# Kernel tuning notes

Hardware: AMD Instinct MI355X
Metric: run time of the kernel (lower is better)

## Reference

```python
import jax, jax.numpy as jnp
import numpy as np

B, N, NP, K, C_IN, C, H = 16, 4096, 1024, 32, 128, 256, 4
C_G = C_IN + 3  # grouped feature dim (use_xyz concat of relative coords)
EPS = 1e-3      # keras LayerNormalization default epsilon


def setup_inputs() -> dict:
    key = jax.random.key(0)
    ks = jax.random.split(key, 16)
    s = 0.05
    return {
        "xyz": jax.random.normal(ks[0], (B, N, 3), jnp.float32),
        "newxyz": jax.random.normal(ks[1], (B, NP, 3), jnp.float32),
        "feature_input": jax.random.normal(ks[2], (B, N, C_IN), jnp.float32),
        "w_qkv": jax.random.normal(ks[3], (C_G, 3 * C), jnp.float32) * s,
        "proj_w": jax.random.normal(ks[4], (C, C), jnp.float32) * s,
        "proj_b": jnp.zeros((C,), jnp.float32),
        "dense_w": jax.random.normal(ks[5], (C_G, C), jnp.float32) * s,
        "dense_b": jnp.zeros((C,), jnp.float32),
        "fc1_w": jax.random.normal(ks[6], (C, 2 * C), jnp.float32) * s,
        "fc1_b": jnp.zeros((2 * C,), jnp.float32),
        "fc2_w": jax.random.normal(ks[7], (2 * C, C), jnp.float32) * s,
        "fc2_b": jnp.zeros((C,), jnp.float32),
        "n1_g": jnp.ones((C_G,), jnp.float32),
        "n1_b": jnp.zeros((C_G,), jnp.float32),
        "n2_g": jnp.ones((C,), jnp.float32),
        "n2_b": jnp.zeros((C,), jnp.float32),
        "group_num": K,
        "training": True,
    }


def _layernorm(x, g, b):
    m = jnp.mean(x, axis=-1, keepdims=True)
    v = jnp.mean(jnp.square(x - m), axis=-1, keepdims=True)
    return (x - m) * jax.lax.rsqrt(v + EPS) * g + b


def _sample_and_group(newxyz, group_num, xyz, feats):
    # squared pairwise distances (B, NP, N)
    d2 = (jnp.sum(newxyz**2, -1)[:, :, None]
          - 2.0 * jnp.einsum('bpc,bnc->bpn', newxyz, xyz)
          + jnp.sum(xyz**2, -1)[:, None, :])
    _, idx = jax.lax.top_k(-d2, group_num)            # (B, NP, K) nearest
    b_idx = jnp.arange(newxyz.shape[0])[:, None, None]
    grouped_xyz = xyz[b_idx, idx] - newxyz[:, :, None, :]   # (B, NP, K, 3)
    grouped_feat = feats[b_idx, idx]                        # (B, NP, K, C_IN)
    return jnp.concatenate([grouped_xyz, grouped_feat], axis=-1)


def _self_attention(x, w_qkv, proj_w, proj_b):
    b, n, k = x.shape[0], x.shape[1], x.shape[2]
    d = C // H
    qkv = jnp.einsum('bnkc,cd->bnkd', x, w_qkv)
    qkv = qkv.reshape(b, n, k, 3, H, d)
    qkv = jnp.transpose(qkv, (3, 0, 1, 4, 2, 5))      # (3, B, NP, H, K, d)
    q, kk, v = qkv[0], qkv[1], qkv[2]
    qm = jnp.max(q, axis=-2, keepdims=True)           # (B, NP, H, 1, d)
    attn = jnp.einsum('bnhqd,bnhkd->bnhqk', qm, kk) * (C ** -0.5)
    attn = jax.nn.softmax(attn, axis=-1)
    out = jnp.einsum('bnhqk,bnhkd->bnhqd', attn, v)[..., 0, :]  # (B, NP, H, d)
    out = out.reshape(b, n, C)
    return jax.nn.relu(out @ proj_w + proj_b)


def reference(xyz, newxyz, feature_input, w_qkv, proj_w, proj_b, dense_w,
              dense_b, fc1_w, fc1_b, fc2_w, fc2_b, n1_g, n1_b, n2_g, n2_b,
              group_num, training):
    gf = _sample_and_group(newxyz, group_num, xyz, feature_input)  # (B,NP,K,C_G)
    feat = _self_attention(_layernorm(gf, n1_g, n1_b), w_qkv, proj_w, proj_b)
    feat = feat + jax.nn.relu(jnp.max(gf, axis=-2) @ dense_w + dense_b)
    f2 = _layernorm(feat, n2_g, n2_b)
    f2 = jax.nn.relu(f2 @ fc1_w + fc1_b)
    f2 = f2 @ fc2_w + fc2_b
    return f2 + feat
```

## Files before the change

kernel.cpp:

```cpp
#include <hip/hip_runtime.h>
#include <hip/hip_bf16.h>

typedef __hip_bfloat16 bf16;

#define Bn   16
#define Nn   4096
#define NPn  1024
#define Kn   32
#define CINn 128
#define CGn  131
#define Cn   256
#define Hn   4
#define KPAD 160
#define XBS  168
#define XFS2 136
#define GFS  136

typedef __attribute__((ext_vector_type(8))) short frag_ab;
typedef __attribute__((ext_vector_type(4))) float frag_cd;

__device__ __forceinline__ float b2f(bf16 x) { return __bfloat162float(x); }
__device__ __forceinline__ bf16  f2b(float x) { return __float2bfloat16(x); }
__device__ __forceinline__ short f2bs(float x) {
  union { bf16 h; short s; } u; u.h = __float2bfloat16(x); return u.s;
}
__device__ __forceinline__ float bs2f(short s) {
  union { short v; bf16 h; } u; u.v = s; return __bfloat162float(u.h);
}
__device__ __forceinline__ unsigned f2ord(float f) {
  unsigned u = __float_as_uint(f);
  return u ^ ((u >> 31) ? 0xffffffffu : 0x80000000u);
}

__global__ __launch_bounds__(256) void knn_kernel(const float* __restrict__ xyz,
                                                  const float* __restrict__ newxyz,
                                                  int* __restrict__ idx_out) {
  constexpr int CAP = 2048;
  __shared__ unsigned long long tmin[256];
  __shared__ __align__(16) unsigned long long cand[CAP + 4];
  __shared__ unsigned long long wtau[4];
  __shared__ unsigned long long wred[4];
  __shared__ int scnt;
  const int bp  = blockIdx.x;
  const int b   = bp >> 10;
  const int tid = threadIdx.x;
  const float qx = newxyz[bp*3 + 0];
  const float qy = newxyz[bp*3 + 1];
  const float qz = newxyz[bp*3 + 2];
  const float sn = __fadd_rn(__fadd_rn(__fmul_rn(qx,qx), __fmul_rn(qy,qy)),
                             __fmul_rn(qz,qz));
  const float* xb = xyz + (size_t)b * Nn * 3;
  unsigned long long key[16];
  unsigned long long lmin = ~0ull;
  #pragma unroll
  for (int s = 0; s < 16; ++s) {
    const int n = s*256 + tid;
    const float xx = xb[n*3 + 0];
    const float xy = xb[n*3 + 1];
    const float xz = xb[n*3 + 2];
    const float sx  = __fadd_rn(__fadd_rn(__fmul_rn(xx,xx), __fmul_rn(xy,xy)),
                                __fmul_rn(xz,xz));
    const float dot = __fadd_rn(__fadd_rn(__fmul_rn(qx,xx), __fmul_rn(qy,xy)),
                                __fmul_rn(qz,xz));
    const float d2 = __fadd_rn(__fsub_rn(sn, __fmul_rn(2.0f, dot)), sx);
    key[s] = ((unsigned long long)f2ord(d2) << 32) | (unsigned)n;
    if (key[s] < lmin) lmin = key[s];
  }
  const int lane = tid & 63, wv = tid >> 6;

  if (tid == 0) scnt = 0;
  tmin[tid] = lmin;
  __syncthreads();

  {
    const unsigned long long* wt = &tmin[wv * 64];
    int rk = 0;
    #pragma unroll 8
    for (int j = 0; j < 64; ++j) rk += (wt[j] < lmin) ? 1 : 0;
    if (rk == 31) wtau[wv] = lmin;
  }
  __syncthreads();
  unsigned long long tau = wtau[0];
  if (wtau[1] < tau) tau = wtau[1];
  if (wtau[2] < tau) tau = wtau[2];
  if (wtau[3] < tau) tau = wtau[3];

  #pragma unroll
  for (int s = 0; s < 16; ++s) {
    if (key[s] <= tau) {
      const int p = atomicAdd(&scnt, 1);
      if (p < CAP) cand[p] = key[s];
    }
  }
  __syncthreads();
  const int m = scnt;

  if (m <= CAP) {
    if (tid < 4) cand[m + tid] = ~0ull;
    __syncthreads();
    const int m4 = (m + 3) & ~3;
    for (int t = tid; t < m; t += 256) {
      const unsigned long long mykey = cand[t];
      int r = 0;
      for (int j = 0; j < m4; j += 4) {
        r += (cand[j+0] < mykey) ? 1 : 0;
        r += (cand[j+1] < mykey) ? 1 : 0;
        r += (cand[j+2] < mykey) ? 1 : 0;
        r += (cand[j+3] < mykey) ? 1 : 0;
      }
      if (r < Kn) idx_out[(size_t)bp*Kn + r] = (int)(mykey & 0xffffffffu);
    }
  } else {
    for (int s = 0; s < Kn; ++s) {
      unsigned long long mm = lmin;
      #pragma unroll
      for (int d = 32; d; d >>= 1) {
        const unsigned lo = __shfl_xor((unsigned)(mm & 0xffffffffu), d, 64);
        const unsigned hi = __shfl_xor((unsigned)(mm >> 32), d, 64);
        const unsigned long long o = ((unsigned long long)hi << 32) | lo;
        if (o < mm) mm = o;
      }
      if (lane == 0) wred[wv] = mm;
      __syncthreads();
      unsigned long long best = wred[0];
      if (wred[1] < best) best = wred[1];
      if (wred[2] < best) best = wred[2];
      if (wred[3] < best) best = wred[3];
      __syncthreads();
      const int n = (int)(best & 0xffffffffu);
      if (tid == 0) idx_out[(size_t)bp*Kn + s] = n;
      if ((n & 255) == tid) {
        const int slot = n >> 8;
        #pragma unroll
        for (int t = 0; t < 16; ++t) if (t == slot) key[t] = ~0ull;
        unsigned long long m2 = ~0ull;
        #pragma unroll
        for (int t = 0; t < 16; ++t) if (key[t] < m2) m2 = key[t];
        lmin = m2;
      }
    }
  }
}

__global__ __launch_bounds__(256) void wprep_all_kernel(
    const float* __restrict__ w_qkv, const float* __restrict__ proj_w,
    const float* __restrict__ dense_w, const float* __restrict__ fc1_w,
    const float* __restrict__ fc2_w, short* __restrict__ o_qkv,
    short* __restrict__ o_proj, short* __restrict__ o_dense,
    short* __restrict__ o_fc1, short* __restrict__ o_fc2) {
  const int blk = blockIdx.x;
  const float* W; short* out; int K, N, nnt, remap, base;
  if      (blk <  480) { W=w_qkv;   out=o_qkv;   K=CGn; N=768; nnt=48; remap=1; base=0;    }
  else if (blk <  736) { W=proj_w;  out=o_proj;  K=Cn;  N=256; nnt=16; remap=0; base=480;  }
  else if (blk <  896) { W=dense_w; out=o_dense; K=CGn; N=256; nnt=16; remap=1; base=736;  }
  else if (blk < 1408) { W=fc1_w;   out=o_fc1;   K=Cn;  N=512; nnt=32; remap=0; base=896;  }
  else                 { W=fc2_w;   out=o_fc2;   K=512; N=256; nnt=16; remap=0; base=1408; }
  const int t = (blk - base) * 256 + threadIdx.x;
  const int j    = t & 7;
  const int lane = (t >> 3) & 63;
  const int nt   = (t >> 9) % nnt;
  const int kt   = (t >> 9) / nnt;
  const int k = kt*32 + (lane >> 4)*8 + j;
  const int n = nt*16 + (lane & 15);
  int krow = k;
  if (remap) krow = (k < 128) ? k + 3 : k - 128;
  out[t] = (k < K) ? f2bs(W[(size_t)krow*N + n]) : (short)0;
}

__global__ __launch_bounds__(256, 3) void fused_attn_kernel(
    const float* __restrict__ xyz, const float* __restrict__ newxyz,
    const float* __restrict__ featin, const short* __restrict__ wfrag,
    const float* __restrict__ n1g, const float* __restrict__ n1b,
    const int* __restrict__ idx, bf16* __restrict__ attnout,
    bf16* __restrict__ gfmax) {
  __shared__ __align__(16) short Xs[64 * XBS];
  __shared__ float sg[CGn], sb[CGn];
  __shared__ int sidx[64];
  const int bp0 = blockIdx.x * 2;
  const int b   = bp0 >> 10;
  const int tid = threadIdx.x;
  if (tid < 64) {
    int n = idx[(size_t)bp0*Kn + tid];
    sidx[tid] = ((unsigned)n < (unsigned)Nn) ? n : 0;
  }
  if (tid < CGn) {
    const int rj = (tid < 128) ? tid + 3 : tid - 128;
    sg[tid] = n1g[rj];
    sb[tid] = n1b[rj];
  }
  __syncthreads();
  const int kk = tid >> 3, sub = tid & 7;
  float4 r[2][4];
  float ex[2] = {0.f, 0.f};
  #pragma unroll
  for (int p = 0; p < 2; ++p) {
    const int row = p*32 + kk;
    const float* frow = featin + ((size_t)b*Nn + sidx[row])*CINn;
    #pragma unroll
    for (int i = 0; i < 4; ++i) r[p][i] = *(const float4*)(frow + sub*4 + 32*i);
    if (sub < 3)
      ex[p] = xyz[((size_t)b*Nn + sidx[row])*3 + sub] - newxyz[(bp0+p)*3 + sub];
  }
  #pragma unroll
  for (int p = 0; p < 2; ++p) {
    const int row = p*32 + kk;
    #pragma unroll
    for (int i = 0; i < 4; ++i) {
      short4 s4 = { f2bs(r[p][i].x), f2bs(r[p][i].y), f2bs(r[p][i].z), f2bs(r[p][i].w) };
      *(short4*)&Xs[row*XFS2 + sub*4 + 32*i] = s4;
    }
    if (sub < 3) Xs[row*XFS2 + 128 + sub] = f2bs(ex[p]);
  }
  float mean[2], rstd[2];
  #pragma unroll
  for (int p = 0; p < 2; ++p) {
    float s = ex[p], s2 = ex[p]*ex[p];
    #pragma unroll
    for (int i = 0; i < 4; ++i) {
      s  += r[p][i].x + r[p][i].y + r[p][i].z + r[p][i].w;
      s2 += r[p][i].x*r[p][i].x + r[p][i].y*r[p][i].y
          + r[p][i].z*r[p][i].z + r[p][i].w*r[p][i].w;
    }
    s  += __shfl_xor(s, 1, 64);  s  += __shfl_xor(s, 2, 64);  s  += __shfl_xor(s, 4, 64);
    s2 += __shfl_xor(s2, 1, 64); s2 += __shfl_xor(s2, 2, 64); s2 += __shfl_xor(s2, 4, 64);
    mean[p] = s * (1.0f/CGn);
    const float var = s2 * (1.0f/CGn) - mean[p]*mean[p];
    rstd[p] = rsqrtf(var + 1e-3f);
  }
  __syncthreads();
  #pragma unroll
  for (int p = 0; p < 2; ++p) {
    if (tid < GFS) {
      float m = 0.f;
      if (tid < CGn) {
        m = -1e30f;
        #pragma unroll
        for (int k2 = 0; k2 < Kn; ++k2)
          m = fmaxf(m, bs2f(Xs[(p*32 + k2)*XFS2 + tid]));
      }
      gfmax[(size_t)(bp0+p)*GFS + tid] = f2b(m);
    }
  }
  __syncthreads();
  #pragma unroll
  for (int p = 0; p < 2; ++p) {
    const int row = p*32 + kk;
    #pragma unroll
    for (int i = 0; i < 4; ++i) {
      const float4 g4 = *(const float4*)&sg[sub*4 + 32*i];
      const float4 b4 = *(const float4*)&sb[sub*4 + 32*i];
      short4 s4;
      s4.x = f2bs((r[p][i].x - mean[p])*rstd[p]*g4.x + b4.x);
      s4.y = f2bs((r[p][i].y - mean[p])*rstd[p]*g4.y + b4.y);
      s4.z = f2bs((r[p][i].z - mean[p])*rstd[p]*g4.z + b4.z);
      s4.w = f2bs((r[p][i].w - mean[p])*rstd[p]*g4.w + b4.w);
      *(short4*)&Xs[row*XBS + sub*4 + 32*i] = s4;
    }
    if (sub < 3)
      Xs[row*XBS + 128 + sub] = f2bs((ex[p] - mean[p])*rstd[p]*sg[128+sub] + sb[128+sub]);
  }
  #pragma unroll
  for (int u = 0; u < 8; ++u) {
    const int e = u*256 + tid;
    const int row = e >> 5, jj = 131 + (e & 31);
    if (jj < 160) Xs[row*XBS + jj] = 0;
  }
  __syncthreads();
  const int lane = tid & 63, w = tid >> 6;
  const int col = lane & 15, quad = lane >> 4;
  float qm[2][4], aw[2][2][4], inv[2];
  {
    #pragma unroll 1
    for (int half = 0; half < 2; ++half) {
      frag_cd acc[2][4] = {};
      for (int kt = 0; kt < 5; ++kt) {
        const int ko = kt*32 + quad*8;
        frag_ab a[4];
        #pragma unroll
        for (int mt = 0; mt < 4; ++mt)
          a[mt] = *(const frag_ab*)&Xs[(mt*16 + col)*XBS + ko];
        #pragma unroll
        for (int ntl = 0; ntl < 2; ++ntl) {
          const int nt = w*4 + half*2 + ntl;
          const frag_ab bfr = *(const frag_ab*)(wfrag + ((size_t)(kt*48 + nt)*64 + lane)*8);
          #pragma unroll
          for (int mt = 0; mt < 4; ++mt)
            acc[ntl][mt] = __builtin_amdgcn_mfma_f32_16x16x32_bf16(a[mt], bfr, acc[ntl][mt], 0, 0, 0);
        }
      }
      #pragma unroll
      for (int p = 0; p < 2; ++p)
        #pragma unroll
        for (int ntl = 0; ntl < 2; ++ntl) {
          float m = -1e30f;
          #pragma unroll
          for (int mtl = 0; mtl < 2; ++mtl)
            #pragma unroll
            for (int rr = 0; rr < 4; ++rr) m = fmaxf(m, acc[ntl][p*2+mtl][rr]);
          m = fmaxf(m, __shfl_xor(m, 16, 64));
          m = fmaxf(m, __shfl_xor(m, 32, 64));
          qm[p][half*2 + ntl] = m;
        }
    }
  }
  {
    float pp[2][2][4] = {};
    #pragma unroll 1
    for (int half = 0; half < 2; ++half) {
      frag_cd acc[2][4] = {};
      for (int kt = 0; kt < 5; ++kt) {
        const int ko = kt*32 + quad*8;
        frag_ab a[4];
        #pragma unroll
        for (int mt = 0; mt < 4; ++mt)
          a[mt] = *(const frag_ab*)&Xs[(mt*16 + col)*XBS + ko];
        #pragma unroll
        for (int ntl = 0; ntl < 2; ++ntl) {
          const int nt = 16 + w*4 + half*2 + ntl;
          const frag_ab bfr = *(const frag_ab*)(wfrag + ((size_t)(kt*48 + nt)*64 + lane)*8);
          #pragma unroll
          for (int mt = 0; mt < 4; ++mt)
            acc[ntl][mt] = __builtin_amdgcn_mfma_f32_16x16x32_bf16(a[mt], bfr, acc[ntl][mt], 0, 0, 0);
        }
      }
      #pragma unroll
      for (int p = 0; p < 2; ++p)
        #pragma unroll
        for (int mtl = 0; mtl < 2; ++mtl)
          #pragma unroll
          for (int rr = 0; rr < 4; ++rr) {
            #pragma unroll
            for (int ntl = 0; ntl < 2; ++ntl)
              pp[p][mtl][rr] = fmaf(qm[p][half*2 + ntl], acc[ntl][p*2+mtl][rr], pp[p][mtl][rr]);
          }
    }
    #pragma unroll
    for (int p = 0; p < 2; ++p) {
      float lg[2][4];
      #pragma unroll
      for (int mtl = 0; mtl < 2; ++mtl)
        #pragma unroll
        for (int rr = 0; rr < 4; ++rr) {
          float v = pp[p][mtl][rr];
          #pragma unroll
          for (int d = 1; d < 16; d <<= 1) v += __shfl_xor(v, d, 64);
          lg[mtl][rr] = v * 0.0625f;
        }
      float mx = -1e30f;
      #pragma unroll
      for (int mtl = 0; mtl < 2; ++mtl)
        #pragma unroll
        for (int rr = 0; rr < 4; ++rr) mx = fmaxf(mx, lg[mtl][rr]);
      mx = fmaxf(mx, __shfl_xor(mx, 16, 64));
      mx = fmaxf(mx, __shfl_xor(mx, 32, 64));
      float ssum = 0.f;
      #pragma unroll
      for (int mtl = 0; mtl < 2; ++mtl)
        #pragma unroll
        for (int rr = 0; rr < 4; ++rr) { aw[p][mtl][rr] = expf(lg[mtl][rr] - mx); ssum += aw[p][mtl][rr]; }
      ssum += __shfl_xor(ssum, 16, 64);
      ssum += __shfl_xor(ssum, 32, 64);
      inv[p] = 1.f / ssum;
    }
  }
  {
    #pragma unroll 1
    for (int half = 0; half < 2; ++half) {
      frag_cd acc[2][4] = {};
      for (int kt = 0; kt < 5; ++kt) {
        const int ko = kt*32 + quad*8;
        frag_ab a[4];
        #pragma unroll
        for (int mt = 0; mt < 4; ++mt)
          a[mt] = *(const frag_ab*)&Xs[(mt*16 + col)*XBS + ko];
        #pragma unroll
        for (int ntl = 0; ntl < 2; ++ntl) {
          const int nt = 32 + w*4 + half*2 + ntl;
          const frag_ab bfr = *(const frag_ab*)(wfrag + ((size_t)(kt*48 + nt)*64 + lane)*8);
          #pragma unroll
          for (int mt = 0; mt < 4; ++mt)
            acc[ntl][mt] = __builtin_amdgcn_mfma_f32_16x16x32_bf16(a[mt], bfr, acc[ntl][mt], 0, 0, 0);
        }
      }
      #pragma unroll
      for (int p = 0; p < 2; ++p)
        #pragma unroll
        for (int ntl = 0; ntl < 2; ++ntl) {
          float o = 0.f;
          #pragma unroll
          for (int mtl = 0; mtl < 2; ++mtl)
            #pragma unroll
            for (int rr = 0; rr < 4; ++rr) o = fmaf(aw[p][mtl][rr], acc[ntl][p*2+mtl][rr], o);
          o += __shfl_xor(o, 16, 64);
          o += __shfl_xor(o, 32, 64);
          if (quad == 0)
            attnout[(size_t)(bp0+p)*Cn + w*64 + (half*2 + ntl)*16 + col] = f2b(o * inv[p]);
        }
    }
  }
}

template<bool RELU, bool ADD_S, bool OUT_BF16>
__global__ __launch_bounds__(256) void mfma_gemm_kernel(
    const bf16* __restrict__ A, int lda, int Ka,
    const short* __restrict__ Wf, int nnt_total, int N,
    const float* __restrict__ bias, const bf16* __restrict__ S,
    void* __restrict__ Dv) {
  __shared__ __align__(16) short As[64*40];
  const int m0 = blockIdx.y * 64;
  const int n0 = blockIdx.x * 128;
  const int tid = threadIdx.x, lane = tid & 63, w = tid >> 6;
  const int col = lane & 15, quad = lane >> 4;
  const int row = tid >> 2, c8 = (tid & 3) * 8;
  frag_cd acc[4][2] = {};
  const int nkt = (Ka + 31) >> 5;
  for (int kt = 0; kt < nkt; ++kt) {
    const int k0 = kt*32 + c8;
    frag_ab av = {0,0,0,0,0,0,0,0};
    if (k0 + 8 <= Ka)
      av = *(const frag_ab*)((const short*)A + (size_t)(m0+row)*lda + k0);
    __syncthreads();
    *(frag_ab*)&As[row*40 + c8] = av;
    __syncthreads();
    frag_ab afr[4];
    #pragma unroll
    for (int mt = 0; mt < 4; ++mt)
      afr[mt] = *(const frag_ab*)&As[(mt*16 + col)*40 + quad*8];
    #pragma unroll
    for (int ntl = 0; ntl < 2; ++ntl) {
      const int nt = (n0 >> 4) + w*2 + ntl;
      const frag_ab bfr = *(const frag_ab*)(Wf + ((size_t)(kt*nnt_total + nt)*64 + lane)*8);
      #pragma unroll
      for (int mt = 0; mt < 4; ++mt)
        acc[mt][ntl] = __builtin_amdgcn_mfma_f32_16x16x32_bf16(afr[mt], bfr, acc[mt][ntl], 0, 0, 0);
    }
  }
  #pragma unroll
  for (int ntl = 0; ntl < 2; ++ntl) {
    const int n = n0 + w*32 + ntl*16 + col;
    const float bv = bias[n];
    #pragma unroll
    for (int mt = 0; mt < 4; ++mt) {
      #pragma unroll
      for (int r = 0; r < 4; ++r) {
        const int m = m0 + mt*16 + quad*4 + r;
        float v = acc[mt][ntl][r] + bv;
        if (RELU) v = fmaxf(v, 0.f);
        if (ADD_S) v += b2f(S[(size_t)m*N + n]);
        if (OUT_BF16) ((bf16*)Dv)[(size_t)m*N + n] = f2b(v);
        else          ((float*)Dv)[(size_t)m*N + n] = v;
      }
    }
  }
}

__global__ __launch_bounds__(256) void dual_gemm_kernel(
    const bf16* __restrict__ A1, const short* __restrict__ W1,
    const bf16* __restrict__ A2, const short* __restrict__ W2,
    const float* __restrict__ b1, const float* __restrict__ b2,
    bf16* __restrict__ D) {
  __shared__ __align__(16) short As[64*40];
  const int m0 = blockIdx.y * 64;
  const int n0 = blockIdx.x * 128;
  const int tid = threadIdx.x, lane = tid & 63, w = tid >> 6;
  const int col = lane & 15, quad = lane >> 4;
  const int row = tid >> 2, c8 = (tid & 3) * 8;
  frag_cd acc1[4][2] = {}, acc2[4][2] = {};
  for (int kt = 0; kt < 8; ++kt) {
    const frag_ab av = *(const frag_ab*)((const short*)A1 + (size_t)(m0+row)*Cn + kt*32 + c8);
    __syncthreads();
    *(frag_ab*)&As[row*40 + c8] = av;
    __syncthreads();
    frag_ab afr[4];
    #pragma unroll
    for (int mt = 0; mt < 4; ++mt)
      afr[mt] = *(const frag_ab*)&As[(mt*16 + col)*40 + quad*8];
    #pragma unroll
    for (int ntl = 0; ntl < 2; ++ntl) {
      const int nt = (n0 >> 4) + w*2 + ntl;
      const frag_ab bfr = *(const frag_ab*)(W1 + ((size_t)(kt*16 + nt)*64 + lane)*8);
      #pragma unroll
      for (int mt = 0; mt < 4; ++mt)
        acc1[mt][ntl] = __builtin_amdgcn_mfma_f32_16x16x32_bf16(afr[mt], bfr, acc1[mt][ntl], 0, 0, 0);
    }
  }
  for (int kt = 0; kt < 5; ++kt) {
    const int k0 = kt*32 + c8;
    frag_ab av = {0,0,0,0,0,0,0,0};
    if (k0 + 8 <= GFS)
      av = *(const frag_ab*)((const short*)A2 + (size_t)(m0+row)*GFS + k0);
    __syncthreads();
    *(frag_ab*)&As[row*40 + c8] = av;
    __syncthreads();
    frag_ab afr[4];
    #pragma unroll
    for (int mt = 0; mt < 4; ++mt)
      afr[mt] = *(const frag_ab*)&As[(mt*16 + col)*40 + quad*8];
    #pragma unroll
    for (int ntl = 0; ntl < 2; ++ntl) {
      const int nt = (n0 >> 4) + w*2 + ntl;
      const frag_ab bfr = *(const frag_ab*)(W2 + ((size_t)(kt*16 + nt)*64 + lane)*8);
      #pragma unroll
      for (int mt = 0; mt < 4; ++mt)
        acc2[mt][ntl] = __builtin_amdgcn_mfma_f32_16x16x32_bf16(afr[mt], bfr, acc2[mt][ntl], 0, 0, 0);
    }
  }
  #pragma unroll
  for (int ntl = 0; ntl < 2; ++ntl) {
    const int n = n0 + w*32 + ntl*16 + col;
    const float bv1 = b1[n], bv2 = b2[n];
    #pragma unroll
    for (int mt = 0; mt < 4; ++mt) {
      #pragma unroll
      for (int r = 0; r < 4; ++r) {
        const int m = m0 + mt*16 + quad*4 + r;
        const float v = fmaxf(acc1[mt][ntl][r] + bv1, 0.f)
                      + fmaxf(acc2[mt][ntl][r] + bv2, 0.f);
        D[(size_t)m*Cn + n] = f2b(v);
      }
    }
  }
}

__global__ __launch_bounds__(256) void ln2_kernel(const bf16* __restrict__ feat,
                                                  const float* __restrict__ g,
                                                  const float* __restrict__ b,
                                                  bf16* __restrict__ out) {
  const int r = blockIdx.x*4 + (threadIdx.x >> 6), lane = threadIdx.x & 63;
  float vv[4];
  #pragma unroll
  for (int c = 0; c < 4; ++c) vv[c] = b2f(feat[(size_t)r*Cn + lane*4 + c]);
  float s  = vv[0] + vv[1] + vv[2] + vv[3];
  float s2 = vv[0]*vv[0] + vv[1]*vv[1] + vv[2]*vv[2] + vv[3]*vv[3];
  #pragma unroll
  for (int d = 32; d; d >>= 1) { s += __shfl_xor(s, d, 64); s2 += __shfl_xor(s2, d, 64); }
  const float mean = s * (1.f/256.f);
  const float var  = s2 * (1.f/256.f) - mean*mean;
  const float rstd = rsqrtf(var + 1e-3f);
  #pragma unroll
  for (int c = 0; c < 4; ++c) {
    const int cc = lane*4 + c;
    out[(size_t)r*Cn + cc] = f2b((vv[c] - mean)*rstd*g[cc] + b[cc]);
  }
}

extern "C" void kernel_launch(void* const* d_in, const int* in_sizes, int n_in,
                              void* d_out, int out_size, void* d_ws, size_t ws_size,
                              hipStream_t stream) {
  const float* xyz     = (const float*)d_in[0];
  const float* newxyz  = (const float*)d_in[1];
  const float* featin  = (const float*)d_in[2];
  const float* w_qkv   = (const float*)d_in[3];
  const float* proj_w  = (const float*)d_in[4];
  const float* proj_b  = (const float*)d_in[5];
  const float* dense_w = (const float*)d_in[6];
  const float* dense_b = (const float*)d_in[7];
  const float* fc1_w   = (const float*)d_in[8];
  const float* fc1_b   = (const float*)d_in[9];
  const float* fc2_w   = (const float*)d_in[10];
  const float* fc2_b   = (const float*)d_in[11];
  const float* n1g     = (const float*)d_in[12];
  const float* n1b     = (const float*)d_in[13];
  const float* n2g     = (const float*)d_in[14];
  const float* n2b     = (const float*)d_in[15];

  char*  ws     = (char*)d_ws;
  short* wqkv   = (short*)(ws + 0);
  short* wproj  = (short*)(ws + 245760);
  short* wdense = (short*)(ws + 376832);
  short* wfc1   = (short*)(ws + 458752);
  short* wfc2   = (short*)(ws + 720896);
  bf16*  featB  = (bf16*)(ws + 1048576);
  bf16*  attnA  = (bf16*)(ws + 9437184);
  bf16*  gfmax  = (bf16*)(ws + 17825792);
  int*   idxws  = (int*) (ws + 22282240);
  bf16*  fc1out = (bf16*)(ws + 24379392);

  const int M = Bn * NPn;

  knn_kernel<<<dim3(M), dim3(256), 0, stream>>>(xyz, newxyz, idxws);
  wprep_all_kernel<<<dim3(1920), dim3(256), 0, stream>>>(
      w_qkv, proj_w, dense_w, fc1_w, fc2_w, wqkv, wproj, wdense, wfc1, wfc2);

  fused_attn_kernel<<<dim3(M/2), dim3(256), 0, stream>>>(
      xyz, newxyz, featin, wqkv, n1g, n1b, idxws, attnA, gfmax);
  dual_gemm_kernel<<<dim3(2, M/64), dim3(256), 0, stream>>>(
      attnA, wproj, gfmax, wdense, proj_b, dense_b, featB);
  ln2_kernel<<<dim3(M/4), dim3(256), 0, stream>>>(featB, n2g, n2b, attnA);
  mfma_gemm_kernel<true, false, true><<<dim3(4, M/64), dim3(256), 0, stream>>>(
      attnA, Cn, Cn, wfc1, 32, 512, fc1_b, (const bf16*)nullptr, fc1out);
  mfma_gemm_kernel<false, true, false><<<dim3(2, M/64), dim3(256), 0, stream>>>(
      fc1out, 512, 512, wfc2, 16, Cn, fc2_b, featB, d_out);
}
```

Before: 435.3 us.

## Precompute padded xyz with squared norms, tighten KNN threshold, stage raw features in LDS

Adds a prep kernel that packs xyz into float4 with the precomputed squared norm, so each KNN block does one vector load per point and skips the norm arithmetic. The KNN candidate threshold now uses the rank-15 thread minimum per wave instead of rank-31, which shrinks the candidate set, and a fallback path handles the case where fewer than K candidates survive. The fused attention kernel keeps the raw bf16 features in a separate LDS buffer instead of holding fp32 registers across barriers, which drops one barrier but adds LDS use and lowers LayerNorm input precision to bf16. The xyzw buffer reuses the fc1out workspace region.

```diff
diff --git a/kernel.cpp b/kernel.cpp
--- a/kernel.cpp
+++ b/kernel.cpp
@@ -32,7 +32,18 @@
   return u ^ ((u >> 31) ? 0xffffffffu : 0x80000000u);
 }
 
-__global__ __launch_bounds__(256) void knn_kernel(const float* __restrict__ xyz,
+__global__ __launch_bounds__(256) void xyzw_prep_kernel(
+    const float* __restrict__ xyz, float4* __restrict__ xyzw) {
+  const int i = blockIdx.x * 256 + threadIdx.x;
+  const float x = xyz[i*3 + 0];
+  const float y = xyz[i*3 + 1];
+  const float z = xyz[i*3 + 2];
+  const float sx = __fadd_rn(__fadd_rn(__fmul_rn(x,x), __fmul_rn(y,y)),
+                             __fmul_rn(z,z));
+  xyzw[i] = make_float4(x, y, z, sx);
+}
+
+__global__ __launch_bounds__(256) void knn_kernel(const float4* __restrict__ xyzw,
                                                   const float* __restrict__ newxyz,
                                                   int* __restrict__ idx_out) {
   constexpr int CAP = 2048;
@@ -49,20 +60,16 @@
   const float qz = newxyz[bp*3 + 2];
   const float sn = __fadd_rn(__fadd_rn(__fmul_rn(qx,qx), __fmul_rn(qy,qy)),
                              __fmul_rn(qz,qz));
-  const float* xb = xyz + (size_t)b * Nn * 3;
+  const float4* xb = xyzw + (size_t)b * Nn;
   unsigned long long key[16];
   unsigned long long lmin = ~0ull;
   #pragma unroll
   for (int s = 0; s < 16; ++s) {
     const int n = s*256 + tid;
-    const float xx = xb[n*3 + 0];
-    const float xy = xb[n*3 + 1];
-    const float xz = xb[n*3 + 2];
-    const float sx  = __fadd_rn(__fadd_rn(__fmul_rn(xx,xx), __fmul_rn(xy,xy)),
-                                __fmul_rn(xz,xz));
-    const float dot = __fadd_rn(__fadd_rn(__fmul_rn(qx,xx), __fmul_rn(qy,xy)),
-                                __fmul_rn(qz,xz));
-    const float d2 = __fadd_rn(__fsub_rn(sn, __fmul_rn(2.0f, dot)), sx);
+    const float4 xw = xb[n];
+    const float dot = __fadd_rn(__fadd_rn(__fmul_rn(qx,xw.x), __fmul_rn(qy,xw.y)),
+                                __fmul_rn(qz,xw.z));
+    const float d2 = __fadd_rn(__fsub_rn(sn, __fmul_rn(2.0f, dot)), xw.w);
     key[s] = ((unsigned long long)f2ord(d2) << 32) | (unsigned)n;
     if (key[s] < lmin) lmin = key[s];
   }
@@ -77,7 +84,7 @@
     int rk = 0;
     #pragma unroll 8
     for (int j = 0; j < 64; ++j) rk += (wt[j] < lmin) ? 1 : 0;
-    if (rk == 31) wtau[wv] = lmin;
+    if (rk == 15) wtau[wv] = lmin;
   }
   __syncthreads();
   unsigned long long tau = wtau[0];
@@ -95,7 +102,7 @@
   __syncthreads();
   const int m = scnt;
 
-  if (m <= CAP) {
+  if (m >= Kn && m <= CAP) {
     if (tid < 4) cand[m + tid] = ~0ull;
     __syncthreads();
     const int m4 = (m + 3) & ~3;
@@ -173,6 +180,7 @@
     const float* __restrict__ n1g, const float* __restrict__ n1b,
     const int* __restrict__ idx, bf16* __restrict__ attnout,
     bf16* __restrict__ gfmax) {
+  __shared__ __align__(16) short Raw[64 * XFS2];
   __shared__ __align__(16) short Xs[64 * XBS];
   __shared__ float sg[CGn], sb[CGn];
   __shared__ int sidx[64];
@@ -190,42 +198,46 @@
   }
   __syncthreads();
   const int kk = tid >> 3, sub = tid & 7;
-  float4 r[2][4];
-  float ex[2] = {0.f, 0.f};
-  #pragma unroll
-  for (int p = 0; p < 2; ++p) {
-    const int row = p*32 + kk;
-    const float* frow = featin + ((size_t)b*Nn + sidx[row])*CINn;
-    #pragma unroll
-    for (int i = 0; i < 4; ++i) r[p][i] = *(const float4*)(frow + sub*4 + 32*i);
-    if (sub < 3)
-      ex[p] = xyz[((size_t)b*Nn + sidx[row])*3 + sub] - newxyz[(bp0+p)*3 + sub];
-  }
-  #pragma unroll
-  for (int p = 0; p < 2; ++p) {
-    const int row = p*32 + kk;
-    #pragma unroll
-    for (int i = 0; i < 4; ++i) {
-      short4 s4 = { f2bs(r[p][i].x), f2bs(r[p][i].y), f2bs(r[p][i].z), f2bs(r[p][i].w) };
-      *(short4*)&Xs[row*XFS2 + sub*4 + 32*i] = s4;
-    }
-    if (sub < 3) Xs[row*XFS2 + 128 + sub] = f2bs(ex[p]);
-  }
+  const int lane = tid & 63, w = tid >> 6;
+  const int col = lane & 15, quad = lane >> 4;
   float mean[2], rstd[2];
-  #pragma unroll
-  for (int p = 0; p < 2; ++p) {
-    float s = ex[p], s2 = ex[p]*ex[p];
-    #pragma unroll
-    for (int i = 0; i < 4; ++i) {
-      s  += r[p][i].x + r[p][i].y + r[p][i].z + r[p][i].w;
-      s2 += r[p][i].x*r[p][i].x + r[p][i].y*r[p][i].y
-          + r[p][i].z*r[p][i].z + r[p][i].w*r[p][i].w;
-    }
-    s  += __shfl_xor(s, 1, 64);  s  += __shfl_xor(s, 2, 64);  s  += __shfl_xor(s, 4, 64);
-    s2 += __shfl_xor(s2, 1, 64); s2 += __shfl_xor(s2, 2, 64); s2 += __shfl_xor(s2, 4, 64);
-    mean[p] = s * (1.0f/CGn);
-    const float var = s2 * (1.0f/CGn) - mean[p]*mean[p];
-    rstd[p] = rsqrtf(var + 1e-3f);
+  {
+    float4 r[2][4];
+    float ex[2] = {0.f, 0.f};
+    #pragma unroll
+    for (int p = 0; p < 2; ++p) {
+      const int row = p*32 + kk;
+      const float* frow = featin + ((size_t)b*Nn + sidx[row])*CINn;
+      #pragma unroll
+      for (int i = 0; i < 4; ++i) r[p][i] = *(const float4*)(frow + sub*4 + 32*i);
+      if (sub < 3)
+        ex[p] = xyz[((size_t)b*Nn + sidx[row])*3 + sub] - newxyz[(bp0+p)*3 + sub];
+    }
+    #pragma unroll
+    for (int p = 0; p < 2; ++p) {
+      const int row = p*32 + kk;
+      #pragma unroll
+      for (int i = 0; i < 4; ++i) {
+        short4 s4 = { f2bs(r[p][i].x), f2bs(r[p][i].y), f2bs(r[p][i].z), f2bs(r[p][i].w) };
+        *(short4*)&Raw[row*XFS2 + sub*4 + 32*i] = s4;
+      }
+      if (sub < 3) Raw[row*XFS2 + 128 + sub] = f2bs(ex[p]);
+    }
+    #pragma unroll
+    for (int p = 0; p < 2; ++p) {
+      float s = ex[p], s2 = ex[p]*ex[p];
+      #pragma unroll
+      for (int i = 0; i < 4; ++i) {
+        s  += r[p][i].x + r[p][i].y + r[p][i].z + r[p][i].w;
+        s2 += r[p][i].x*r[p][i].x + r[p][i].y*r[p][i].y
+            + r[p][i].z*r[p][i].z + r[p][i].w*r[p][i].w;
+      }
+      s  += __shfl_xor(s, 1, 64);  s  += __shfl_xor(s, 2, 64);  s  += __shfl_xor(s, 4, 64);
+      s2 += __shfl_xor(s2, 1, 64); s2 += __shfl_xor(s2, 2, 64); s2 += __shfl_xor(s2, 4, 64);
+      mean[p] = s * (1.0f/CGn);
+      const float var = s2 * (1.0f/CGn) - mean[p]*mean[p];
+      rstd[p] = rsqrtf(var + 1e-3f);
+    }
   }
   __syncthreads();
   #pragma unroll
@@ -236,12 +248,11 @@
         m = -1e30f;
         #pragma unroll
         for (int k2 = 0; k2 < Kn; ++k2)
-          m = fmaxf(m, bs2f(Xs[(p*32 + k2)*XFS2 + tid]));
+          m = fmaxf(m, bs2f(Raw[(p*32 + k2)*XFS2 + tid]));
       }
       gfmax[(size_t)(bp0+p)*GFS + tid] = f2b(m);
     }
   }
-  __syncthreads();
   #pragma unroll
   for (int p = 0; p < 2; ++p) {
     const int row = p*32 + kk;
@@ -249,15 +260,18 @@
     for (int i = 0; i < 4; ++i) {
       const float4 g4 = *(const float4*)&sg[sub*4 + 32*i];
       const float4 b4 = *(const float4*)&sb[sub*4 + 32*i];
+      const short4 rv = *(const short4*)&Raw[row*XFS2 + sub*4 + 32*i];
       short4 s4;
-      s4.x = f2bs((r[p][i].x - mean[p])*rstd[p]*g4.x + b4.x);
-      s4.y = f2bs((r[p][i].y - mean[p])*rstd[p]*g4.y + b4.y);
-      s4.z = f2bs((r[p][i].z - mean[p])*rstd[p]*g4.z + b4.z);
-      s4.w = f2bs((r[p][i].w - mean[p])*rstd[p]*g4.w + b4.w);
+      s4.x = f2bs((bs2f(rv.x) - mean[p])*rstd[p]*g4.x + b4.x);
+      s4.y = f2bs((bs2f(rv.y) - mean[p])*rstd[p]*g4.y + b4.y);
+      s4.z = f2bs((bs2f(rv.z) - mean[p])*rstd[p]*g4.z + b4.z);
+      s4.w = f2bs((bs2f(rv.w) - mean[p])*rstd[p]*g4.w + b4.w);
       *(short4*)&Xs[row*XBS + sub*4 + 32*i] = s4;
     }
-    if (sub < 3)
-      Xs[row*XBS + 128 + sub] = f2bs((ex[p] - mean[p])*rstd[p]*sg[128+sub] + sb[128+sub]);
+    if (sub < 3) {
+      const float rxv = bs2f(Raw[row*XFS2 + 128 + sub]);
+      Xs[row*XBS + 128 + sub] = f2bs((rxv - mean[p])*rstd[p]*sg[128+sub] + sb[128+sub]);
+    }
   }
   #pragma unroll
   for (int u = 0; u < 8; ++u) {
@@ -266,8 +280,6 @@
     if (jj < 160) Xs[row*XBS + jj] = 0;
   }
   __syncthreads();
-  const int lane = tid & 63, w = tid >> 6;
-  const int col = lane & 15, quad = lane >> 4;
   float qm[2][4], aw[2][2][4], inv[2];
   {
     #pragma unroll 1
@@ -575,10 +587,12 @@
   bf16*  gfmax  = (bf16*)(ws + 17825792);
   int*   idxws  = (int*) (ws + 22282240);
   bf16*  fc1out = (bf16*)(ws + 24379392);
+  float4* xyzw  = (float4*)(ws + 24379392);
 
   const int M = Bn * NPn;
 
-  knn_kernel<<<dim3(M), dim3(256), 0, stream>>>(xyz, newxyz, idxws);
+  xyzw_prep_kernel<<<dim3(Bn*Nn/256), dim3(256), 0, stream>>>(xyz, xyzw);
+  knn_kernel<<<dim3(M), dim3(256), 0, stream>>>(xyzw, newxyz, idxws);
   wprep_all_kernel<<<dim3(1920), dim3(256), 0, stream>>>(
       w_qkv, proj_w, dense_w, fc1_w, fc2_w, wqkv, wproj, wdense, wfc1, wfc2);
 
```

New measurement: 421.2 us. 1.03x faster.
